# Kernel tuning notes

Measured on AMD Instinct MI355X. Metric: run time of the kernel, lower is better.

Reference implementation:

```python
import jax, jax.numpy as jnp
import numpy as np

N = 100_000   # nodes
E = 1_600_000 # directed edges
G = 2048      # graphs in batch
NF = 78       # input node features
DIM = 32      # GIN hidden dim
L = 5         # num GIN layers
OUT = 128     # output_dim
BN_EPS = 1e-5


def setup_inputs() -> dict:
    key = jax.random.key(0)
    ks = jax.random.split(key, 8)
    s = 0.1
    return {
        "x": jax.random.normal(ks[0], (N, NF), jnp.float32),
        "edge_index": jax.random.randint(ks[1], (2, E), 0, N, jnp.int32),
        "batch": jnp.sort(jax.random.randint(ks[2], (N,), 0, G, jnp.int32)),
        "W1_0": (jax.random.normal(ks[3], (NF, DIM), jnp.float32) * s),
        "W1_rest": (jax.random.normal(ks[4], (L - 1, DIM, DIM), jnp.float32) * s),
        "b1": jnp.zeros((L, DIM), jnp.float32),
        "W2": (jax.random.normal(ks[5], (L, DIM, DIM), jnp.float32) * s),
        "b2": jnp.zeros((L, DIM), jnp.float32),
        "gamma": jnp.ones((L, DIM), jnp.float32),
        "beta": jnp.zeros((L, DIM), jnp.float32),
        "Wfc": (jax.random.normal(ks[6], (DIM, OUT), jnp.float32) * s),
        "bfc": jnp.zeros((OUT,), jnp.float32),
    }


def reference(x, edge_index, batch, W1_0, W1_rest, b1, W2, b2, gamma, beta, Wfc, bfc):
    src, dst = edge_index[0], edge_index[1]
    h = x
    for i in range(L):
        # GINConv (eps=0): h_i' = MLP(h_i + sum_{j->i} h_j)
        agg = jax.ops.segment_sum(h[src], dst, num_segments=N)  # [N, d]
        h = h + agg
        W1 = W1_0 if i == 0 else W1_rest[i - 1]
        h = jnp.maximum(h @ W1 + b1[i], 0.0) @ W2[i] + b2[i]
        # ReLU then BatchNorm1d (training mode: batch stats, biased var)
        h = jnp.maximum(h, 0.0)
        mu = h.mean(axis=0)
        var = h.var(axis=0)
        h = gamma[i] * (h - mu) * jax.lax.rsqrt(var + BN_EPS) + beta[i]
    pooled = jax.ops.segment_sum(h, batch, num_segments=G)  # global_add_pool [G, DIM]
    return jnp.maximum(pooled @ Wfc + bfc, 0.0)  # dropout is identity (eval)
```

## Files before the change

kernel.cpp:

```cpp
#include <hip/hip_runtime.h>
#include <hip/hip_fp16.h>

#define N_NODES 100000
#define N_EDGES 1600000
#define N_GRAPHS 2048
#define NFEAT 78
#define DIM 32
#define NLAYERS 5
#define OUTD 128
#define BN_EPS 1e-5f
#define NPB 32
#define NBUK 391
#define BNODES 256
#define STRIDE 4608
#define EPB 4096
#define NBLK ((N_EDGES + EPB - 1) / EPB)
#define NSLOTS2 ((N_NODES / NPB + 63) / 64)

__device__ __forceinline__ float2 up2(unsigned u) {
    __half2 h = *reinterpret_cast<__half2*>(&u);
    return __half22float2(h);
}
__device__ __forceinline__ unsigned pk2(float a, float b) {
    __half2 h = __floats2half2_rn(a, b);
    return *reinterpret_cast<unsigned*>(&h);
}

__global__ __launch_bounds__(256) void prep_kernel(
    const int* __restrict__ ei, int* __restrict__ bcnt, int* __restrict__ bdata,
    const float* __restrict__ x, const float* __restrict__ W1_0,
    unsigned short* __restrict__ y)
{
    __shared__ int cur[NBUK];
    __shared__ int gbl[NBUK];
    __shared__ float Wl[NFEAT * DIM];
    int tid = threadIdx.x;

    if (blockIdx.x < NBLK) {
        int base = blockIdx.x * EPB;
        for (int i = tid; i < NBUK; i += 256) cur[i] = 0;
        __syncthreads();

        int ew[16], eb[16];
        const int4* s4 = (const int4*)ei;
        const int4* d4 = (const int4*)(ei + N_EDGES);
#pragma unroll
        for (int c = 0; c < 4; ++c) {
            int eidx = base + c * 1024 + tid * 4;
            if (eidx < N_EDGES) {
                int4 sv = s4[eidx >> 2];
                int4 dv = d4[eidx >> 2];
                ew[c*4+0] = sv.x | ((dv.x & 255) << 17); eb[c*4+0] = dv.x >> 8;
                ew[c*4+1] = sv.y | ((dv.y & 255) << 17); eb[c*4+1] = dv.y >> 8;
                ew[c*4+2] = sv.z | ((dv.z & 255) << 17); eb[c*4+2] = dv.z >> 8;
                ew[c*4+3] = sv.w | ((dv.w & 255) << 17); eb[c*4+3] = dv.w >> 8;
            } else {
                eb[c*4+0] = eb[c*4+1] = eb[c*4+2] = eb[c*4+3] = -1;
                ew[c*4+0] = ew[c*4+1] = ew[c*4+2] = ew[c*4+3] = 0;
            }
        }
        int slot[16];
#pragma unroll
        for (int k = 0; k < 16; ++k)
            slot[k] = (eb[k] >= 0) ? atomicAdd(&cur[eb[k]], 1) : 0;
        __syncthreads();
        for (int b = tid; b < NBUK; b += 256) {
            int c = cur[b];
            gbl[b] = (c > 0) ? atomicAdd(&bcnt[b], c) : 0;
        }
        __syncthreads();
#pragma unroll
        for (int k = 0; k < 16; ++k) {
            int b = eb[k];
            if (b >= 0) {
                int pos = gbl[b] + slot[k];
                if (pos < STRIDE) bdata[b * STRIDE + pos] = ew[k];
            }
        }
    } else {
        for (int i = tid; i < NFEAT * DIM; i += 256) Wl[i] = W1_0[i];
        __syncthreads();
        int t = (blockIdx.x - NBLK) * 256 + tid;
        int row = t >> 3;
        int c0 = (t & 7) * 4;
        float a0 = 0.f, a1 = 0.f, a2 = 0.f, a3 = 0.f;
        const float* hr = x + (long)row * NFEAT;
        for (int k = 0; k < NFEAT; ++k) {
            float xv = hr[k];
            a0 = fmaf(xv, Wl[k * DIM + c0 + 0], a0);
            a1 = fmaf(xv, Wl[k * DIM + c0 + 1], a1);
            a2 = fmaf(xv, Wl[k * DIM + c0 + 2], a2);
            a3 = fmaf(xv, Wl[k * DIM + c0 + 3], a3);
        }
        ((uint2*)y)[(long)row * 8 + (t & 7)] = make_uint2(pk2(a0, a1), pk2(a2, a3));
    }
}

__global__ __launch_bounds__(512) void bscan_kernel(
    const int* __restrict__ bcnt, int* __restrict__ bbase)
{
    __shared__ int sd[512];
    int t = threadIdx.x;
    int v = (t < NBUK) ? min(bcnt[t], STRIDE) : 0;
    sd[t] = v; __syncthreads();
    for (int off = 1; off < 512; off <<= 1) {
        int a = (t >= off) ? sd[t - off] : 0;
        __syncthreads();
        sd[t] += a;
        __syncthreads();
    }
    if (t < NBUK) bbase[t + 1] = sd[t];
    if (t == 0) bbase[0] = 0;
}

__global__ __launch_bounds__(256) void cfill2_kernel(
    const int* __restrict__ bcnt, const int* __restrict__ bbase,
    const int* __restrict__ bdata, int* __restrict__ edge_src,
    int* __restrict__ offs)
{
    __shared__ int sorted[STRIDE];
    __shared__ int cnt[BNODES], off[BNODES], cur[BNODES];
    int b = blockIdx.x, tid = threadIdx.x;
    int n = min(bcnt[b], STRIDE);
    int gb = bbase[b];
    const int* slab = bdata + (long)b * STRIDE;

    if (tid < BNODES) cnt[tid] = 0;
    __syncthreads();
    for (int i = tid; i < n; i += 256)
        atomicAdd(&cnt[slab[i] >> 17], 1);
    __syncthreads();
    int t = tid;
    if (t < BNODES) off[t] = cnt[t];
    __syncthreads();
    for (int o = 1; o < BNODES; o <<= 1) {
        int a = (t >= o && t < BNODES) ? off[t - o] : 0;
        __syncthreads();
        if (t < BNODES) off[t] += a;
        __syncthreads();
    }
    if (t < BNODES) {
        int excl = off[t] - cnt[t];
        off[t] = excl;
        cur[t] = excl;
        int node = b * BNODES + t;
        if (node <= N_NODES) offs[node] = gb + excl;
    }
    __syncthreads();
    for (int i = tid; i < n; i += 256) {
        int w = slab[i];
        int pos = atomicAdd(&cur[w >> 17], 1);
        sorted[pos] = w & 0x1FFFF;
    }
    __syncthreads();
    for (int i = tid; i < n; i += 256)
        edge_src[gb + i] = sorted[i];
}

template<bool MM>
__global__ __launch_bounds__(256) void layer_kernel(
    const int* __restrict__ offs, const int* __restrict__ edge_src,
    const unsigned short* __restrict__ zin,
    const float* __restrict__ W1g,
    const float* __restrict__ partial_prev,
    const float* __restrict__ gprev, const float* __restrict__ bprev,
    const float* __restrict__ b1v,
    const float* __restrict__ W2, const float* __restrict__ b2v,
    unsigned short* __restrict__ zout, float* __restrict__ partial)
{
    __shared__ float W1l[DIM * DIM];
    __shared__ float W2l[DIM * DIM];
    __shared__ float zs[NPB][36];
    __shared__ float b1l[DIM], b2l[DIM], cl[DIM];
    __shared__ float sscl[DIM], sshl[DIM];
    __shared__ float psum[DIM], psq[DIM];

    int tid = threadIdx.x;
    float* red = &zs[0][0];

    for (int i = tid; i < DIM * DIM; i += 256) W2l[i] = W2[i];
    if (tid < DIM) {
        b1l[tid] = b1v[tid]; b2l[tid] = b2v[tid];
        psum[tid] = 0.f; psq[tid] = 0.f;
    }
    if (MM) {
        int c = tid & 63, chunk = tid >> 6;
        float a = 0.f;
        for (int p = chunk; p < NSLOTS2; p += 4) a += partial_prev[p * 64 + c];
        red[tid] = a;
        __syncthreads();
        if (tid < 64) red[tid] = red[tid] + red[tid+64] + red[tid+128] + red[tid+192];
        __syncthreads();
        if (tid < DIM) {
            const float invN = 1.0f / (float)N_NODES;
            float S = red[tid], Q = red[tid + DIM];
            float mu = S * invN;
            float var = Q * invN - mu * mu;
            float sc = gprev[tid] * rsqrtf(var + BN_EPS);
            sscl[tid] = sc;
            sshl[tid] = bprev[tid] - mu * sc;
        }
        __syncthreads();
        for (int i = tid; i < DIM * DIM; i += 256) W1l[i] = sscl[i >> 5] * W1g[i];
        if (tid < DIM) {
            float cv = 0.f;
            for (int k = 0; k < DIM; ++k) cv = fmaf(sshl[k], W1g[k * DIM + tid], cv);
            cl[tid] = cv;
        }
    }
    __syncthreads();

    int ln = tid >> 3, p = tid & 7;
    int c0 = p * 4;
    long node = (long)blockIdx.x * NPB + ln;
    int beg = offs[node], end = offs[node + 1];
    int deg = end - beg;
    const uint2* zb = (const uint2*)zin;

    uint2 sv = zb[node * 8 + p];
    float2 f;
    f = up2(sv.x); float a0 = f.x, a1 = f.y;
    f = up2(sv.y); float a2 = f.x, a3 = f.y;
    int e = beg;
    for (; e + 8 <= end; e += 8) {
        uint2 v0 = zb[(long)edge_src[e + 0] * 8 + p];
        uint2 v1 = zb[(long)edge_src[e + 1] * 8 + p];
        uint2 v2 = zb[(long)edge_src[e + 2] * 8 + p];
        uint2 v3 = zb[(long)edge_src[e + 3] * 8 + p];
        uint2 v4 = zb[(long)edge_src[e + 4] * 8 + p];
        uint2 v5 = zb[(long)edge_src[e + 5] * 8 + p];
        uint2 v6 = zb[(long)edge_src[e + 6] * 8 + p];
        uint2 v7 = zb[(long)edge_src[e + 7] * 8 + p];
        f = up2(v0.x); a0 += f.x; a1 += f.y;  f = up2(v0.y); a2 += f.x; a3 += f.y;
        f = up2(v1.x); a0 += f.x; a1 += f.y;  f = up2(v1.y); a2 += f.x; a3 += f.y;
        f = up2(v2.x); a0 += f.x; a1 += f.y;  f = up2(v2.y); a2 += f.x; a3 += f.y;
        f = up2(v3.x); a0 += f.x; a1 += f.y;  f = up2(v3.y); a2 += f.x; a3 += f.y;
        f = up2(v4.x); a0 += f.x; a1 += f.y;  f = up2(v4.y); a2 += f.x; a3 += f.y;
        f = up2(v5.x); a0 += f.x; a1 += f.y;  f = up2(v5.y); a2 += f.x; a3 += f.y;
        f = up2(v6.x); a0 += f.x; a1 += f.y;  f = up2(v6.y); a2 += f.x; a3 += f.y;
        f = up2(v7.x); a0 += f.x; a1 += f.y;  f = up2(v7.y); a2 += f.x; a3 += f.y;
    }
    for (; e < end; ++e) {
        uint2 v = zb[(long)edge_src[e] * 8 + p];
        f = up2(v.x); a0 += f.x; a1 += f.y;
        f = up2(v.y); a2 += f.x; a3 += f.y;
    }
    *(float4*)&zs[ln][c0] = make_float4(a0, a1, a2, a3);

    float t4[4];
    if (MM) {
        t4[0] = t4[1] = t4[2] = t4[3] = 0.f;
#pragma unroll
        for (int k = 0; k < DIM; ++k) {
            float zk = zs[ln][k];
            t4[0] = fmaf(zk, W1l[k * DIM + c0 + 0], t4[0]);
            t4[1] = fmaf(zk, W1l[k * DIM + c0 + 1], t4[1]);
            t4[2] = fmaf(zk, W1l[k * DIM + c0 + 2], t4[2]);
            t4[3] = fmaf(zk, W1l[k * DIM + c0 + 3], t4[3]);
        }
        float dp1 = (float)(deg + 1);
#pragma unroll
        for (int j = 0; j < 4; ++j)
            t4[j] = fmaxf(fmaf(dp1, cl[c0 + j], t4[j]) + b1l[c0 + j], 0.f);
    } else {
        t4[0] = fmaxf(a0 + b1l[c0 + 0], 0.f);
        t4[1] = fmaxf(a1 + b1l[c0 + 1], 0.f);
        t4[2] = fmaxf(a2 + b1l[c0 + 2], 0.f);
        t4[3] = fmaxf(a3 + b1l[c0 + 3], 0.f);
    }
    *(float4*)&zs[ln][c0] = make_float4(t4[0], t4[1], t4[2], t4[3]);

    float zv[4] = { b2l[c0 + 0], b2l[c0 + 1], b2l[c0 + 2], b2l[c0 + 3] };
#pragma unroll
    for (int k = 0; k < DIM; ++k) {
        float sk = zs[ln][k];
        zv[0] = fmaf(sk, W2l[k * DIM + c0 + 0], zv[0]);
        zv[1] = fmaf(sk, W2l[k * DIM + c0 + 1], zv[1]);
        zv[2] = fmaf(sk, W2l[k * DIM + c0 + 2], zv[2]);
        zv[3] = fmaf(sk, W2l[k * DIM + c0 + 3], zv[3]);
    }
#pragma unroll
    for (int j = 0; j < 4; ++j) zv[j] = fmaxf(zv[j], 0.f);
    ((uint2*)zout)[node * 8 + p] = make_uint2(pk2(zv[0], zv[1]), pk2(zv[2], zv[3]));

    float sq[4];
#pragma unroll
    for (int j = 0; j < 4; ++j) sq[j] = zv[j] * zv[j];
#pragma unroll
    for (int off = 8; off < 64; off <<= 1) {
#pragma unroll
        for (int j = 0; j < 4; ++j) {
            zv[j] += __shfl_xor(zv[j], off, 64);
            sq[j] += __shfl_xor(sq[j], off, 64);
        }
    }
    if ((tid & 63) < 8) {
#pragma unroll
        for (int j = 0; j < 4; ++j) {
            atomicAdd(&psum[c0 + j], zv[j]);
            atomicAdd(&psq[c0 + j], sq[j]);
        }
    }
    __syncthreads();
    if (tid < 2 * DIM) {
        float v = (tid < DIM) ? psum[tid] : psq[tid - DIM];
        atomicAdd(&partial[(long)(blockIdx.x >> 6) * 2 * DIM + tid], v);
    }
}

__global__ __launch_bounds__(256) void pool_kernel(
    const unsigned short* __restrict__ z, const int* __restrict__ batch,
    float* __restrict__ praw, float* __restrict__ cntg)
{
    __shared__ float acc[32][32];
    __shared__ float cntL[32];
    __shared__ int slot[32];
    __shared__ int segg[32];
    __shared__ int nsegS;
    int tid = threadIdx.x;
    for (int i = tid; i < 1024; i += 256) ((float*)acc)[i] = 0.f;
    if (tid < 32) cntL[tid] = 0.f;
    int nodeBase = blockIdx.x * 32;
    if (tid < 32) {
        int nd = nodeBase + tid;
        int gv = batch[nd];
        int flag = (tid == 0) ? 1 : (gv != batch[nd - 1]);
        unsigned long long m = __ballot(flag);
        int s = __popcll(m & ((2ull << tid) - 1ull)) - 1;
        slot[tid] = s;
        if (flag) segg[s] = gv;
        if (tid == 0) nsegS = __popcll(m);
    }
    __syncthreads();

    int ln = tid >> 3;
    int p = tid & 7;
    long node = nodeBase + ln;
    uint2 u = ((const uint2*)z)[node * 8 + p];
    int c = p * 4;
    float2 f01 = up2(u.x), f23 = up2(u.y);
    int s = slot[ln];
    atomicAdd(&acc[s][c+0], f01.x);
    atomicAdd(&acc[s][c+1], f01.y);
    atomicAdd(&acc[s][c+2], f23.x);
    atomicAdd(&acc[s][c+3], f23.y);
    if (p == 0) atomicAdd(&cntL[s], 1.f);
    __syncthreads();

    int total = nsegS * 32;
    for (int i = tid; i < total; i += 256) {
        int r = i >> 5, dd = i & 31;
        float val = acc[r][dd];
        if (val != 0.f) atomicAdd(&praw[(long)segg[r] * DIM + dd], val);
    }
    if (tid < nsegS) atomicAdd(&cntg[segg[tid]], cntL[tid]);
}

__global__ __launch_bounds__(256) void fc_kernel(
    const float* __restrict__ praw, const float* __restrict__ cntg,
    const float* __restrict__ partial4,
    const float* __restrict__ g4, const float* __restrict__ be4,
    const float* __restrict__ Wfc, const float* __restrict__ bfc,
    float* __restrict__ out)
{
    __shared__ float Wl[DIM * OUTD];
    __shared__ float red[256];
    __shared__ float sscl[DIM], sshl[DIM], dvec[OUTD];
    int tid = threadIdx.x;
    for (int i = tid; i < DIM * OUTD; i += 256) Wl[i] = Wfc[i];
    {
        int c = tid & 63, chunk = tid >> 6;
        float a = 0.f;
        for (int p = chunk; p < NSLOTS2; p += 4) a += partial4[p * 64 + c];
        red[tid] = a;
    }
    __syncthreads();
    if (tid < 64) red[tid] = red[tid] + red[tid+64] + red[tid+128] + red[tid+192];
    __syncthreads();
    if (tid < DIM) {
        const float invN = 1.0f / (float)N_NODES;
        float S = red[tid], Q = red[tid + DIM];
        float mu = S * invN;
        float var = Q * invN - mu * mu;
        float sc = g4[tid] * rsqrtf(var + BN_EPS);
        sscl[tid] = sc;
        sshl[tid] = be4[tid] - mu * sc;
    }
    __syncthreads();
    if (tid < OUTD) {
        float dv = 0.f;
        for (int k = 0; k < DIM; ++k) dv = fmaf(sshl[k], Wl[k * OUTD + tid], dv);
        dvec[tid] = dv;
    }
    __syncthreads();
    int t = blockIdx.x * 256 + tid;
    int g = t >> 7;
    int o = t & (OUTD - 1);
    float acc = bfc[o] + cntg[g] * dvec[o];
    const float* pr = praw + (long)g * DIM;
#pragma unroll
    for (int k = 0; k < DIM; ++k)
        acc = fmaf(sscl[k] * pr[k], Wl[k * OUTD + o], acc);
    out[t] = fmaxf(acc, 0.f);
}

extern "C" void kernel_launch(void* const* d_in, const int* in_sizes, int n_in,
                              void* d_out, int out_size, void* d_ws, size_t ws_size,
                              hipStream_t stream) {
    const float* x      = (const float*)d_in[0];
    const int*   ei     = (const int*)  d_in[1];
    const int*   batch  = (const int*)  d_in[2];
    const float* W1_0   = (const float*)d_in[3];
    const float* W1_rest= (const float*)d_in[4];
    const float* b1     = (const float*)d_in[5];
    const float* W2     = (const float*)d_in[6];
    const float* b2     = (const float*)d_in[7];
    const float* gamma  = (const float*)d_in[8];
    const float* beta   = (const float*)d_in[9];
    const float* Wfc    = (const float*)d_in[10];
    const float* bfc    = (const float*)d_in[11];
    float* out = (float*)d_out;

    int* wsi = (int*)d_ws;
    const size_t nf = (size_t)N_NODES * DIM;
    const size_t BD = (size_t)NBUK * STRIDE;
    const size_t PSTRIDE = (size_t)NSLOTS2 * 2 * DIM;
    int*   bdata  = wsi;
    unsigned short* zfpA = (unsigned short*)(wsi + BD);
    unsigned short* zfpB = zfpA + nf;
    int*   edge_src = (int*)(zfpB + nf);
    int*   offs   = edge_src + N_EDGES;
    int*   bcnt   = offs + (N_NODES + 1);
    int*   bbase  = bcnt + NBUK;
    float* praw   = (float*)(bbase + NBUK + 1);
    float* cntg   = praw + (size_t)N_GRAPHS * DIM;
    float* partial= cntg + N_GRAPHS;

    hipMemsetAsync(praw, 0,
        ((size_t)N_GRAPHS * DIM + N_GRAPHS + NLAYERS * PSTRIDE) * sizeof(float),
        stream);
    hipMemsetAsync(bcnt, 0, (size_t)NBUK * sizeof(int), stream);

    const int grpBlocks = (N_NODES * 8) / 256;

    prep_kernel<<<NBLK + grpBlocks, 256, 0, stream>>>(
        ei, bcnt, bdata, x, W1_0, zfpA);
    bscan_kernel<<<1, 512, 0, stream>>>(bcnt, bbase);
    cfill2_kernel<<<NBUK, 256, 0, stream>>>(bcnt, bbase, bdata, edge_src, offs);

    layer_kernel<false><<<N_NODES / NPB, 256, 0, stream>>>(
        offs, edge_src, zfpA, nullptr, nullptr, nullptr, nullptr,
        b1, W2, b2, zfpB, partial);

    const unsigned short* zi = zfpB;
    unsigned short* zo = zfpA;
    for (int i = 1; i < NLAYERS; ++i) {
        layer_kernel<true><<<N_NODES / NPB, 256, 0, stream>>>(
            offs, edge_src, zi,
            W1_rest + (size_t)(i - 1) * DIM * DIM,
            partial + (size_t)(i - 1) * PSTRIDE,
            gamma + (i - 1) * DIM, beta + (i - 1) * DIM,
            b1 + i * DIM, W2 + (size_t)i * DIM * DIM, b2 + i * DIM,
            zo, partial + (size_t)i * PSTRIDE);
        const unsigned short* tmp = zi; zi = zo; zo = (unsigned short*)tmp;
    }

    pool_kernel<<<N_NODES / 32, 256, 0, stream>>>(zi, batch, praw, cntg);
    fc_kernel<<<(N_GRAPHS * OUTD) / 256, 256, 0, stream>>>(
        praw, cntg, partial + (size_t)(NLAYERS - 1) * PSTRIDE,
        gamma + (NLAYERS - 1) * DIM, beta + (NLAYERS - 1) * DIM,
        Wfc, bfc, out);
}
```

Measured before the change: 302.4 us.

## Sort nodes by degree for balanced layer blocks and shrink edge-bucket blocks

Adds a degree histogram in the CSR fill, a scan, and a fill kernel that builds a permutation of nodes grouped by in-degree. Layer kernels then process nodes in this order, so the 8-lane groups within a block have similar edge counts and less divergence and tail imbalance. Per-node feature reads and writes become scattered through the permutation, which can hurt coalescing. It also halves edges per prep block and spreads BN-statistic atomics over 16 fixed slots instead of per-64-block slots.

```diff
diff --git a/kernel.cpp b/kernel.cpp
--- a/kernel.cpp
+++ b/kernel.cpp
@@ -13,9 +13,10 @@
 #define NBUK 391
 #define BNODES 256
 #define STRIDE 4608
-#define EPB 4096
+#define EPB 2048
 #define NBLK ((N_EDGES + EPB - 1) / EPB)
-#define NSLOTS2 ((N_NODES / NPB + 63) / 64)
+#define NSLOT 16
+#define PSTRIDE (NSLOT * 2 * DIM)
 
 __device__ __forceinline__ float2 up2(unsigned u) {
     __half2 h = *reinterpret_cast<__half2*>(&u);
@@ -41,11 +42,11 @@
         for (int i = tid; i < NBUK; i += 256) cur[i] = 0;
         __syncthreads();
 
-        int ew[16], eb[16];
+        int ew[8], eb[8];
         const int4* s4 = (const int4*)ei;
         const int4* d4 = (const int4*)(ei + N_EDGES);
 #pragma unroll
-        for (int c = 0; c < 4; ++c) {
+        for (int c = 0; c < 2; ++c) {
             int eidx = base + c * 1024 + tid * 4;
             if (eidx < N_EDGES) {
                 int4 sv = s4[eidx >> 2];
@@ -59,9 +60,9 @@
                 ew[c*4+0] = ew[c*4+1] = ew[c*4+2] = ew[c*4+3] = 0;
             }
         }
-        int slot[16];
-#pragma unroll
-        for (int k = 0; k < 16; ++k)
+        int slot[8];
+#pragma unroll
+        for (int k = 0; k < 8; ++k)
             slot[k] = (eb[k] >= 0) ? atomicAdd(&cur[eb[k]], 1) : 0;
         __syncthreads();
         for (int b = tid; b < NBUK; b += 256) {
@@ -70,7 +71,7 @@
         }
         __syncthreads();
 #pragma unroll
-        for (int k = 0; k < 16; ++k) {
+        for (int k = 0; k < 8; ++k) {
             int b = eb[k];
             if (b >= 0) {
                 int pos = gbl[b] + slot[k];
@@ -116,16 +117,18 @@
 __global__ __launch_bounds__(256) void cfill2_kernel(
     const int* __restrict__ bcnt, const int* __restrict__ bbase,
     const int* __restrict__ bdata, int* __restrict__ edge_src,
-    int* __restrict__ offs)
+    int* __restrict__ offs, int* __restrict__ ghist)
 {
     __shared__ int sorted[STRIDE];
     __shared__ int cnt[BNODES], off[BNODES], cur[BNODES];
+    __shared__ int lhist[64];
     int b = blockIdx.x, tid = threadIdx.x;
     int n = min(bcnt[b], STRIDE);
     int gb = bbase[b];
     const int* slab = bdata + (long)b * STRIDE;
 
     if (tid < BNODES) cnt[tid] = 0;
+    if (tid < 64) lhist[tid] = 0;
     __syncthreads();
     for (int i = tid; i < n; i += 256)
         atomicAdd(&cnt[slab[i] >> 17], 1);
@@ -145,8 +148,13 @@
         cur[t] = excl;
         int node = b * BNODES + t;
         if (node <= N_NODES) offs[node] = gb + excl;
-    }
-    __syncthreads();
+        if (node < N_NODES) atomicAdd(&lhist[min(cnt[t], 63)], 1);
+    }
+    __syncthreads();
+    if (tid < 64) {
+        int h = lhist[tid];
+        if (h) atomicAdd(&ghist[tid], h);
+    }
     for (int i = tid; i < n; i += 256) {
         int w = slab[i];
         int pos = atomicAdd(&cur[w >> 17], 1);
@@ -157,8 +165,52 @@
         edge_src[gb + i] = sorted[i];
 }
 
+__global__ __launch_bounds__(64) void dscan_kernel(
+    const int* __restrict__ ghist, int* __restrict__ binCursor)
+{
+    __shared__ int sd[64];
+    int t = threadIdx.x;
+    int v = ghist[t];
+    sd[t] = v; __syncthreads();
+    for (int off = 1; off < 64; off <<= 1) {
+        int a = (t >= off) ? sd[t - off] : 0;
+        __syncthreads();
+        sd[t] += a;
+        __syncthreads();
+    }
+    binCursor[t] = sd[t] - v;
+}
+
+__global__ __launch_bounds__(256) void dfill_kernel(
+    const int* __restrict__ offs, int* __restrict__ binCursor,
+    int* __restrict__ perm)
+{
+    __shared__ int lhist[64], lbase[64], lcur[64];
+    int tid = threadIdx.x;
+    int node = blockIdx.x * 256 + tid;
+    if (tid < 64) { lhist[tid] = 0; lcur[tid] = 0; }
+    __syncthreads();
+    int bin = -1;
+    if (node < N_NODES) {
+        int d = offs[node + 1] - offs[node];
+        bin = min(d, 63);
+        atomicAdd(&lhist[bin], 1);
+    }
+    __syncthreads();
+    if (tid < 64) {
+        int c = lhist[tid];
+        lbase[tid] = c ? atomicAdd(&binCursor[tid], c) : 0;
+    }
+    __syncthreads();
+    if (bin >= 0) {
+        int p = atomicAdd(&lcur[bin], 1);
+        perm[lbase[bin] + p] = node;
+    }
+}
+
 template<bool MM>
 __global__ __launch_bounds__(256) void layer_kernel(
+    const int* __restrict__ perm,
     const int* __restrict__ offs, const int* __restrict__ edge_src,
     const unsigned short* __restrict__ zin,
     const float* __restrict__ W1g,
@@ -186,7 +238,7 @@
     if (MM) {
         int c = tid & 63, chunk = tid >> 6;
         float a = 0.f;
-        for (int p = chunk; p < NSLOTS2; p += 4) a += partial_prev[p * 64 + c];
+        for (int p = chunk; p < NSLOT; p += 4) a += partial_prev[p * 64 + c];
         red[tid] = a;
         __syncthreads();
         if (tid < 64) red[tid] = red[tid] + red[tid+64] + red[tid+128] + red[tid+192];
@@ -212,12 +264,12 @@
 
     int ln = tid >> 3, p = tid & 7;
     int c0 = p * 4;
-    long node = (long)blockIdx.x * NPB + ln;
+    int node = perm[blockIdx.x * NPB + ln];
     int beg = offs[node], end = offs[node + 1];
     int deg = end - beg;
     const uint2* zb = (const uint2*)zin;
 
-    uint2 sv = zb[node * 8 + p];
+    uint2 sv = zb[(long)node * 8 + p];
     float2 f;
     f = up2(sv.x); float a0 = f.x, a1 = f.y;
     f = up2(sv.y); float a2 = f.x, a3 = f.y;
@@ -281,7 +333,7 @@
     }
 #pragma unroll
     for (int j = 0; j < 4; ++j) zv[j] = fmaxf(zv[j], 0.f);
-    ((uint2*)zout)[node * 8 + p] = make_uint2(pk2(zv[0], zv[1]), pk2(zv[2], zv[3]));
+    ((uint2*)zout)[(long)node * 8 + p] = make_uint2(pk2(zv[0], zv[1]), pk2(zv[2], zv[3]));
 
     float sq[4];
 #pragma unroll
@@ -304,7 +356,7 @@
     __syncthreads();
     if (tid < 2 * DIM) {
         float v = (tid < DIM) ? psum[tid] : psq[tid - DIM];
-        atomicAdd(&partial[(long)(blockIdx.x >> 6) * 2 * DIM + tid], v);
+        atomicAdd(&partial[(blockIdx.x & (NSLOT - 1)) * 2 * DIM + tid], v);
     }
 }
 
@@ -371,7 +423,7 @@
     {
         int c = tid & 63, chunk = tid >> 6;
         float a = 0.f;
-        for (int p = chunk; p < NSLOTS2; p += 4) a += partial4[p * 64 + c];
+        for (int p = chunk; p < NSLOT; p += 4) a += partial4[p * 64 + c];
         red[tid] = a;
     }
     __syncthreads();
@@ -424,14 +476,16 @@
     int* wsi = (int*)d_ws;
     const size_t nf = (size_t)N_NODES * DIM;
     const size_t BD = (size_t)NBUK * STRIDE;
-    const size_t PSTRIDE = (size_t)NSLOTS2 * 2 * DIM;
     int*   bdata  = wsi;
     unsigned short* zfpA = (unsigned short*)(wsi + BD);
     unsigned short* zfpB = zfpA + nf;
     int*   edge_src = (int*)(zfpB + nf);
     int*   offs   = edge_src + N_EDGES;
-    int*   bcnt   = offs + (N_NODES + 1);
-    int*   bbase  = bcnt + NBUK;
+    int*   perm   = offs + (N_NODES + 1);
+    int*   bcnt   = perm + N_NODES;
+    int*   ghist  = bcnt + NBUK;
+    int*   binCursor = ghist + 64;
+    int*   bbase  = binCursor + 64;
     float* praw   = (float*)(bbase + NBUK + 1);
     float* cntg   = praw + (size_t)N_GRAPHS * DIM;
     float* partial= cntg + N_GRAPHS;
@@ -439,24 +493,27 @@
     hipMemsetAsync(praw, 0,
         ((size_t)N_GRAPHS * DIM + N_GRAPHS + NLAYERS * PSTRIDE) * sizeof(float),
         stream);
-    hipMemsetAsync(bcnt, 0, (size_t)NBUK * sizeof(int), stream);
+    hipMemsetAsync(bcnt, 0, (size_t)(NBUK + 64) * sizeof(int), stream);
 
     const int grpBlocks = (N_NODES * 8) / 256;
 
     prep_kernel<<<NBLK + grpBlocks, 256, 0, stream>>>(
         ei, bcnt, bdata, x, W1_0, zfpA);
     bscan_kernel<<<1, 512, 0, stream>>>(bcnt, bbase);
-    cfill2_kernel<<<NBUK, 256, 0, stream>>>(bcnt, bbase, bdata, edge_src, offs);
+    cfill2_kernel<<<NBUK, 256, 0, stream>>>(
+        bcnt, bbase, bdata, edge_src, offs, ghist);
+    dscan_kernel<<<1, 64, 0, stream>>>(ghist, binCursor);
+    dfill_kernel<<<(N_NODES + 255) / 256, 256, 0, stream>>>(offs, binCursor, perm);
 
     layer_kernel<false><<<N_NODES / NPB, 256, 0, stream>>>(
-        offs, edge_src, zfpA, nullptr, nullptr, nullptr, nullptr,
+        perm, offs, edge_src, zfpA, nullptr, nullptr, nullptr, nullptr,
         b1, W2, b2, zfpB, partial);
 
     const unsigned short* zi = zfpB;
     unsigned short* zo = zfpA;
     for (int i = 1; i < NLAYERS; ++i) {
         layer_kernel<true><<<N_NODES / NPB, 256, 0, stream>>>(
-            offs, edge_src, zi,
+            perm, offs, edge_src, zi,
             W1_rest + (size_t)(i - 1) * DIM * DIM,
             partial + (size_t)(i - 1) * PSTRIDE,
             gamma + (i - 1) * DIM, beta + (i - 1) * DIM,
```

After: 315.2 us. 4.2% more time.
